# Kernel optimization log

Measured on AMD Instinct MI355X. Metric: run time of the kernel, lower is better.

Reference implementation:

```python
import jax, jax.numpy as jnp
import numpy as np

V, E, H1, H2, Q = 50257, 128, 128, 64, 64
K_BEAM, T_ENC, MAX_LEN = 10, 2048, 30
SOS, EOS, ALPHA = 1, 2, 1.2
NEG = -1e30


def setup_inputs() -> dict:
    key = jax.random.key(0)
    ks = jax.random.split(key, 16)
    s = 0.05  # scale params so logits stay well-conditioned
    emb = jax.random.normal(ks[3], (V, E), jnp.float32) * s
    emb = emb.at[EOS].set(0.0)  # padding_idx=<eos> row is zeros
    return {
        'enc_key': jax.random.normal(ks[0], (T_ENC, 1, Q), jnp.float32),
        'enc_values': jax.random.normal(ks[1], (T_ENC, 1, Q), jnp.float32),
        'mask': jnp.ones((1, 1, T_ENC), jnp.float32),
        'embedding': emb,
        'W_ih1': jax.random.normal(ks[4], (4 * H1, E + Q), jnp.float32) * s,
        'W_hh1': jax.random.normal(ks[5], (4 * H1, H1), jnp.float32) * s,
        'b_ih1': jax.random.normal(ks[6], (4 * H1,), jnp.float32) * s,
        'b_hh1': jax.random.normal(ks[7], (4 * H1,), jnp.float32) * s,
        'W_ih2': jax.random.normal(ks[8], (4 * H2, H1), jnp.float32) * s,
        'W_hh2': jax.random.normal(ks[9], (4 * H2, H2), jnp.float32) * s,
        'b_ih2': jax.random.normal(ks[10], (4 * H2,), jnp.float32) * s,
        'b_hh2': jax.random.normal(ks[11], (4 * H2,), jnp.float32) * s,
        'Wq': jax.random.normal(ks[12], (Q, H2), jnp.float32) * s,
        'bq': jax.random.normal(ks[13], (Q,), jnp.float32) * s,
        'Wc': jax.random.normal(ks[14], (V, H2 + Q), jnp.float32) * s,
        'bc': jax.random.normal(ks[15], (V,), jnp.float32) * s,
    }


def _lstm_cell(x, h, c, Wih, Whh, bih, bhh):
    # torch LSTMCell gate order: i, f, g, o
    g = x @ Wih.T + bih + h @ Whh.T + bhh
    i, f, gg, o = jnp.split(g, 4, axis=-1)
    c = jax.nn.sigmoid(f) * c + jax.nn.sigmoid(i) * jnp.tanh(gg)
    h = jax.nn.sigmoid(o) * jnp.tanh(c)
    return h, c


def beam_search(enc_key, enc_values, mask, embedding, W_ih1, W_hh1, b_ih1, b_hh1,
                W_ih2, W_hh2, b_ih2, b_hh2, Wq, bq, Wc, bc):
    k = K_BEAM
    key_t = jnp.transpose(jnp.broadcast_to(enc_key, (T_ENC, k, Q)), (1, 0, 2))    # [k,T,Q]
    val_t = jnp.transpose(jnp.broadcast_to(enc_values, (T_ENC, k, Q)), (1, 0, 2))  # [k,T,Q]
    m = jnp.broadcast_to(mask[:, 0, :], (k, T_ENC))                                # [k,T]
    eos_row = jnp.where(jnp.arange(V) == EOS, 0.0, NEG)  # finished beams: force <eos> at logp 0
    beam_ids = jnp.arange(k)

    carry0 = (jnp.full((k,), SOS, jnp.int32),      # prev words
              jnp.zeros((k,), jnp.float32),        # cumulative scores
              jnp.zeros((k, H1)), jnp.zeros((k, H1)),  # lstm1 h,c
              jnp.zeros((k, H2)), jnp.zeros((k, H2)),  # lstm2 h,c
              jnp.zeros((k, Q)),                   # attention context
              jnp.zeros((k,), bool),               # finished mask
              jnp.full((k, MAX_LEN + 1), SOS, jnp.int32))  # seqs buffer

    def step(carry, i):
        prev, scores, h1, c1, h2, c2, ctx, fin, seqs = carry
        emb = embedding[prev]                                   # [k,E]
        h1, c1 = _lstm_cell(jnp.concatenate([emb, ctx], -1), h1, c1, W_ih1, W_hh1, b_ih1, b_hh1)
        h2, c2 = _lstm_cell(h1, h2, c2, W_ih2, W_hh2, b_ih2, b_hh2)
        q = h2 @ Wq.T + bq                                       # [k,Q]
        energy = jnp.einsum('kq,ktq->kt', q, key_t)              # [k,T]
        att = jax.nn.softmax(energy, axis=1)
        matt = m * att
        matt = matt / jnp.clip(matt.sum(axis=1, keepdims=True), 2e-30)
        ctx = jnp.einsum('kt,ktv->kv', matt, val_t)              # [k,Q]
        logits = jnp.concatenate([h2, ctx], -1) @ Wc.T + bc      # [k,V]
        logp = jax.nn.log_softmax(logits, axis=1)
        logp = jnp.where(fin[:, None], eos_row[None, :], logp)
        cand = scores[:, None] + logp                            # [k,V]
        # step 0: all beams identical -> only expand beam 0 (matches scores[0].topk)
        cand = jnp.where((i == 0) & (beam_ids[:, None] > 0), NEG, cand)
        top_scores, top_idx = jax.lax.top_k(cand.reshape(-1), k)
        prev_beam = top_idx // V
        nxt = (top_idx % V).astype(jnp.int32)
        h1, c1, h2, c2, ctx = (a[prev_beam] for a in (h1, c1, h2, c2, ctx))
        seqs = seqs[prev_beam].at[:, i + 1].set(nxt)
        fin = fin[prev_beam] | (nxt == EOS)
        return (nxt, top_scores, h1, c1, h2, c2, ctx, fin, seqs), None

    carry, _ = jax.lax.scan(step, carry0, jnp.arange(MAX_LEN))
    _, scores, _, _, _, _, _, _, seqs = carry
    is_eos = seqs[:, 1:] == EOS
    has_eos = is_eos.any(axis=1)
    first = jnp.argmax(is_eos, axis=1)
    # length = tokens incl. <sos> and <eos> (forced <eos> appended if never produced)
    length = jnp.where(has_eos, first + 2, MAX_LEN + 2).astype(jnp.float32)
    norm_scores = scores / (length ** ALPHA)
    return seqs, scores, norm_scores


def reference(enc_key, enc_values, mask, embedding, W_ih1, W_hh1, b_ih1, b_hh1,
              W_ih2, W_hh2, b_ih2, b_hh2, Wq, bq, Wc, bc):
    return beam_search(enc_key, enc_values, mask, embedding, W_ih1, W_hh1, b_ih1, b_hh1,
                       W_ih2, W_hh2, b_ih2, b_hh2, Wq, bq, Wc, bc)
```

## Files before the change

kernel.cpp:

```cpp
#include <hip/hip_runtime.h>
#include <math.h>

#define K_BEAM  10
#define V_SZ    50257
#define E_SZ    128
#define H1_SZ   128
#define H2_SZ   64
#define Q_SZ    64
#define T_SZ    2048
#define MAXLEN  30
#define SEQ_LEN 31
#define SOS_TOK 1
#define EOS_TOK 2

#define NBLK 256
#define NTHR 512
#define VC   197
#define XSTR 132

#define ST_A_F   0
#define ST_B_F   8960
#define SD_H1    0
#define SD_C1    1280
#define SD_H2    2560
#define SD_C2    3200
#define SD_CTX   3840
#define META_A_F 17920
#define META_B_F 18272
#define M_SC     0
#define M_FIN    20
#define M_PREV   30
#define M_SEQ    40
#define XS_F     19936
#define LSEM_F   83136
#define LSES_F   88256
#define CANDV_F  93376
#define CANDI_F  118976
#define B10V_F   144576
#define B10F_F   144776

__device__ __forceinline__ void wave_merge_ms_d(double& m, double& s) {
  #pragma unroll
  for (int off = 32; off > 0; off >>= 1) {
    double om = __shfl_down(m, off, 64);
    double os = __shfl_down(s, off, 64);
    double nm = fmax(m, om);
    s = s * exp(m - nm) + os * exp(om - nm);
    m = nm;
  }
}
__device__ __forceinline__ void wave_argmax_f(float& v, int& i) {
  #pragma unroll
  for (int off = 32; off > 0; off >>= 1) {
    float ov = __shfl_down(v, off, 64);
    int   oi = __shfl_down(i, off, 64);
    if (ov > v || (ov == v && oi < i)) { v = ov; i = oi; }
  }
}

__device__ __forceinline__ void merge100(const float* ws, double* selv, int* self_, int lane) {
  const double* bv = (const double*)(ws + B10V_F);
  const int*    bf = (const int*)(ws + B10F_F);
  double av = (lane < 100) ? bv[lane] : -1e302;
  int    af = (lane < 100) ? bf[lane] : 0x7fffffff;
  const int c1 = lane + 64;
  double cv = (c1 < 100) ? bv[c1] : -1e302;
  int    cf = (c1 < 100) ? bf[c1] : 0x7fffffff;
  #pragma unroll
  for (int pick = 0; pick < 10; ++pick) {
    bool tb = (cv > av) || (cv == av && cf < af);
    double lv = tb ? cv : av;
    int    lf = tb ? cf : af;
    int    ls = tb ? c1 : lane;
    #pragma unroll
    for (int off = 32; off > 0; off >>= 1) {
      double ov = __shfl_down(lv, off, 64);
      int    of = __shfl_down(lf, off, 64);
      int    os = __shfl_down(ls, off, 64);
      if (ov > lv || (ov == lv && of < lf)) { lv = ov; lf = of; ls = os; }
    }
    ls = __shfl(ls, 0, 64);
    if (lane == 0) { selv[pick] = lv; self_[pick] = lf; }
    if (ls == lane) { av = -1e302; af = 0x7fffffff; }
    if (ls == c1)   { cv = -1e302; cf = 0x7fffffff; }
  }
}

__global__ __launch_bounds__(NTHR, 2) void stepA_kernel(
    float* __restrict__ ws, int step,
    const float* __restrict__ embedding,
    const float* __restrict__ W_ih1, const float* __restrict__ W_hh1,
    const float* __restrict__ b_ih1, const float* __restrict__ b_hh1,
    const float* __restrict__ W_ih2, const float* __restrict__ W_hh2,
    const float* __restrict__ b_ih2, const float* __restrict__ b_hh2,
    const float* __restrict__ Wq, const float* __restrict__ bq,
    const float* __restrict__ enc_key, const float* __restrict__ enc_values,
    const float* __restrict__ maskp)
{
  const int blk = blockIdx.x;
  if (blk & 7) return;
  const int b = blk >> 3;

  const int tid  = threadIdx.x;
  const int lane = tid & 63;
  const int wv   = tid >> 6;

  __shared__ double sh_e[T_SZ];
  __shared__ double sh_red[NTHR];
  __shared__ double sh_xin[192];
  __shared__ double sh_h1p[128];
  __shared__ double sh_g1[512];
  __shared__ double sh_h1n[128];
  __shared__ double sh_h2p[64];
  __shared__ double sh_gt2[256];
  __shared__ double sh_h2n[64];
  __shared__ double sh_qs[64];
  __shared__ double sh_selv[10];
  __shared__ int    sh_self[10];
  __shared__ int    sh_pb, sh_tok;

  const int par = step & 1;
  const double* S = (const double*)(ws + (par == 0 ? ST_A_F : ST_B_F));
  double*       D = (double*)(ws + (par == 0 ? ST_B_F : ST_A_F));
  const float* msrc = ws + (par == 0 ? META_A_F : META_B_F);
  float*       mdst = ws + (par == 0 ? META_B_F : META_A_F);

  if (step == 0) {
    double* SA = (double*)(ws + ST_A_F);
    if (tid < 128) { SA[SD_H1 + b*H1_SZ + tid] = 0.0; SA[SD_C1 + b*H1_SZ + tid] = 0.0; }
    if (tid >= 128 && tid < 192) {
      int i2 = tid - 128;
      SA[SD_H2 + b*H2_SZ + i2] = 0.0; SA[SD_C2 + b*H2_SZ + i2] = 0.0;
      SA[SD_CTX + b*Q_SZ + i2] = 0.0;
    }
    float* mA = ws + META_A_F;
    if (tid == 0) {
      ((double*)(mA + M_SC))[b] = 0.0;
      ((int*)(mA + M_FIN))[b] = 0;
      ((int*)(mA + M_PREV))[b] = SOS_TOK;
    }
    if (tid < SEQ_LEN) ((int*)(mA + M_SEQ))[b*SEQ_LEN + tid] = SOS_TOK;
    __syncthreads();
  }

  if (step == 0) {
    if (tid == 0) {
      int tok = ((const int*)(msrc + M_PREV))[b];
      double sc = ((const double*)(msrc + M_SC))[b];
      int fin = ((const int*)(msrc + M_FIN))[b];
      sh_pb = b; sh_tok = tok;
      ((double*)(mdst + M_SC))[b] = sc;
      ((int*)(mdst + M_FIN))[b] = fin;
      ((int*)(mdst + M_PREV))[b] = tok;
    }
  } else {
    if (wv == 0) merge100(ws, sh_selv, sh_self, lane);
    __syncthreads();
    if (tid == 0) {
      int f = sh_self[b];
      int pb = f / V_SZ; int tok = f - pb*V_SZ;
      pb = min(max(pb, 0), K_BEAM - 1); tok = min(max(tok, 0), V_SZ - 1);
      double sc = sh_selv[b];
      int fin = ((const int*)(msrc + M_FIN))[pb] | (tok == EOS_TOK);
      sh_pb = pb; sh_tok = tok;
      ((double*)(mdst + M_SC))[b] = sc;
      ((int*)(mdst + M_FIN))[b] = fin;
      ((int*)(mdst + M_PREV))[b] = tok;
    }
  }
  __syncthreads();
  const int pb = sh_pb, tok = sh_tok;

  if (tid < SEQ_LEN) {
    int v = ((const int*)(msrc + M_SEQ))[pb*SEQ_LEN + tid];
    if (step > 0 && tid == step) v = tok;
    ((int*)(mdst + M_SEQ))[b*SEQ_LEN + tid] = v;
  }
  if (tid < 128)                     sh_xin[tid] = (double)embedding[(size_t)tok*E_SZ + tid];
  else if (tid < 192)                sh_xin[tid] = S[SD_CTX + pb*Q_SZ + (tid - 128)];
  if (tid >= 256 && tid < 384)       sh_h1p[tid - 256] = S[SD_H1 + pb*H1_SZ + (tid - 256)];
  __syncthreads();

  {
    const int r = tid;
    double acc = (double)b_ih1[r] + (double)b_hh1[r];
    const float4* wi = (const float4*)(W_ih1 + (size_t)r*192);
    float4 st[12];
    for (int j0 = 0; j0 < 48; j0 += 12) {
      #pragma unroll
      for (int u = 0; u < 12; ++u) st[u] = wi[j0 + u];
      #pragma unroll
      for (int u = 0; u < 12; ++u) {
        const int j = j0 + u;
        acc += (double)st[u].x*sh_xin[4*j]   + (double)st[u].y*sh_xin[4*j+1]
             + (double)st[u].z*sh_xin[4*j+2] + (double)st[u].w*sh_xin[4*j+3];
      }
    }
    const float4* wh = (const float4*)(W_hh1 + (size_t)r*128);
    for (int j0 = 0; j0 < 32; j0 += 8) {
      #pragma unroll
      for (int u = 0; u < 8; ++u) st[u] = wh[j0 + u];
      #pragma unroll
      for (int u = 0; u < 8; ++u) {
        const int j = j0 + u;
        acc += (double)st[u].x*sh_h1p[4*j]   + (double)st[u].y*sh_h1p[4*j+1]
             + (double)st[u].z*sh_h1p[4*j+2] + (double)st[u].w*sh_h1p[4*j+3];
      }
    }
    sh_g1[r] = acc;
  }
  __syncthreads();
  if (tid < 128) {
    double ig = 1.0/(1.0 + exp(-sh_g1[tid]));
    double fg = 1.0/(1.0 + exp(-sh_g1[128 + tid]));
    double gg = tanh(sh_g1[256 + tid]);
    double og = 1.0/(1.0 + exp(-sh_g1[384 + tid]));
    double c = fg * S[SD_C1 + pb*H1_SZ + tid] + ig*gg;
    double h = og * tanh(c);
    D[SD_C1 + b*H1_SZ + tid] = c; D[SD_H1 + b*H1_SZ + tid] = h;
    sh_h1n[tid] = h;
  }
  if (tid >= 128 && tid < 192) sh_h2p[tid - 128] = S[SD_H2 + pb*H2_SZ + (tid - 128)];
  __syncthreads();

  if (tid < 256) {
    const int r = tid;
    double acc = (double)b_ih2[r] + (double)b_hh2[r];
    const float4* wi2 = (const float4*)(W_ih2 + (size_t)r*128);
    float4 st[8];
    for (int j0 = 0; j0 < 32; j0 += 8) {
      #pragma unroll
      for (int u = 0; u < 8; ++u) st[u] = wi2[j0 + u];
      #pragma unroll
      for (int u = 0; u < 8; ++u) {
        const int j = j0 + u;
        acc += (double)st[u].x*sh_h1n[4*j]   + (double)st[u].y*sh_h1n[4*j+1]
             + (double)st[u].z*sh_h1n[4*j+2] + (double)st[u].w*sh_h1n[4*j+3];
      }
    }
    const float4* wh2 = (const float4*)(W_hh2 + (size_t)r*64);
    for (int j0 = 0; j0 < 16; j0 += 8) {
      #pragma unroll
      for (int u = 0; u < 8; ++u) st[u] = wh2[j0 + u];
      #pragma unroll
      for (int u = 0; u < 8; ++u) {
        const int j = j0 + u;
        acc += (double)st[u].x*sh_h2p[4*j]   + (double)st[u].y*sh_h2p[4*j+1]
             + (double)st[u].z*sh_h2p[4*j+2] + (double)st[u].w*sh_h2p[4*j+3];
      }
    }
    sh_gt2[r] = acc;
  }
  __syncthreads();
  if (tid < 64) {
    double ig = 1.0/(1.0 + exp(-sh_gt2[tid]));
    double fg = 1.0/(1.0 + exp(-sh_gt2[64 + tid]));
    double gg = tanh(sh_gt2[128 + tid]);
    double og = 1.0/(1.0 + exp(-sh_gt2[192 + tid]));
    double c = fg * S[SD_C2 + pb*H2_SZ + tid] + ig*gg;
    double h = og * tanh(c);
    D[SD_C2 + b*H2_SZ + tid] = c; D[SD_H2 + b*H2_SZ + tid] = h;
    sh_h2n[tid] = h;
    ((double*)(ws + XS_F))[b*128 + tid] = h;
  }
  __syncthreads();
  if (tid < 64) {
    double acc = (double)bq[tid];
    const float4* wr = (const float4*)(Wq + (size_t)tid*64);
    float4 st[16];
    #pragma unroll
    for (int u = 0; u < 16; ++u) st[u] = wr[u];
    #pragma unroll
    for (int j = 0; j < 16; ++j) {
      acc += (double)st[j].x*sh_h2n[4*j]   + (double)st[j].y*sh_h2n[4*j+1]
           + (double)st[j].z*sh_h2n[4*j+2] + (double)st[j].w*sh_h2n[4*j+3];
    }
    sh_qs[tid] = acc;
  }
  __syncthreads();

  double lmax = -1e300;
  for (int t = tid; t < T_SZ; t += NTHR) {
    const float4* kr = (const float4*)(enc_key + (size_t)t*64);
    float4 st[16];
    #pragma unroll
    for (int u = 0; u < 16; ++u) st[u] = kr[u];
    double e = 0.0;
    #pragma unroll
    for (int j = 0; j < 16; ++j) {
      e += (double)st[j].x*sh_qs[4*j]   + (double)st[j].y*sh_qs[4*j+1]
         + (double)st[j].z*sh_qs[4*j+2] + (double)st[j].w*sh_qs[4*j+3];
    }
    sh_e[t] = e;
    lmax = fmax(lmax, e);
  }
  sh_red[tid] = lmax; __syncthreads();
  for (int s2 = 256; s2 > 0; s2 >>= 1) { if (tid < s2) sh_red[tid] = fmax(sh_red[tid], sh_red[tid + s2]); __syncthreads(); }
  const double mx = sh_red[0]; __syncthreads();
  double lsum = 0.0;
  for (int t = tid; t < T_SZ; t += NTHR) lsum += exp(sh_e[t] - mx);
  sh_red[tid] = lsum; __syncthreads();
  for (int s2 = 256; s2 > 0; s2 >>= 1) { if (tid < s2) sh_red[tid] += sh_red[tid + s2]; __syncthreads(); }
  const double Ss = sh_red[0]; __syncthreads();
  double lms = 0.0;
  for (int t = tid; t < T_SZ; t += NTHR) {
    double w = (double)maskp[t] * (exp(sh_e[t] - mx) / Ss);
    sh_e[t] = w;
    lms += w;
  }
  sh_red[tid] = lms; __syncthreads();
  for (int s2 = 256; s2 > 0; s2 >>= 1) { if (tid < s2) sh_red[tid] += sh_red[tid + s2]; __syncthreads(); }
  const double ms = fmax(sh_red[0], 2e-30); __syncthreads();
  {
    const int v = tid & 63, g = tid >> 6;
    double acc = 0.0;
    float ev[8];
    for (int k0 = 0; k0 < 256; k0 += 8) {
      #pragma unroll
      for (int u = 0; u < 8; ++u)
        ev[u] = enc_values[(size_t)(g + 8*(k0 + u))*64 + v];
      #pragma unroll
      for (int u = 0; u < 8; ++u)
        acc += sh_e[g + 8*(k0 + u)] * (double)ev[u];
    }
    sh_red[tid] = acc;
  }
  __syncthreads();
  if (tid < 64) {
    double cv = 0.0;
    #pragma unroll
    for (int g = 0; g < 8; ++g) cv += sh_red[g*64 + tid];
    cv /= ms;
    D[SD_CTX + b*Q_SZ + tid] = cv;
    ((double*)(ws + XS_F))[b*128 + 64 + tid] = cv;
  }
}

__global__ __launch_bounds__(NTHR, 2) void stepB_kernel(
    float* __restrict__ ws, int step,
    const float* __restrict__ Wc, const float* __restrict__ bc)
{
  const int tid  = threadIdx.x;
  const int blk  = blockIdx.x;
  const int lane = tid & 63;
  const int wv   = tid >> 6;

  __shared__ double sh_xs[K_BEAM*XSTR];
  __shared__ float  sh_lg[VC*K_BEAM];

  const int v0 = blk * VC;
  const int vn = min(VC, V_SZ - v0);

  for (int i2 = tid; i2 < K_BEAM*128; i2 += NTHR) {
    int b2 = i2 >> 7, j = i2 & 127;
    sh_xs[b2*XSTR + j] = ((const double*)(ws + XS_F))[i2];
  }
  __syncthreads();

  {
    const int g = lane >> 3, k = lane & 7;
    for (int r0 = wv * 8; r0 < vn; r0 += 64) {
      const int r = r0 + g;
      const bool act = (r < vn);
      float4 rw0, rw1, rw2, rw3;
      double bcv = 0.0;
      if (act) {
        const float4* wr4 = (const float4*)(Wc + (size_t)(v0 + r)*128);
        rw0 = wr4[k]; rw1 = wr4[k + 8]; rw2 = wr4[k + 16]; rw3 = wr4[k + 24];
        bcv = (double)bc[v0 + r];
      } else {
        rw0 = rw1 = rw2 = rw3 = make_float4(0.f, 0.f, 0.f, 0.f);
      }
      #pragma unroll 1
      for (int b2 = 0; b2 < K_BEAM; ++b2) {
        const double* xb = &sh_xs[b2*XSTR];
        double p = 0.0;
        {
          const double* xp = xb + (k + 0)*4;
          p += (double)rw0.x*xp[0]; p += (double)rw0.y*xp[1];
          p += (double)rw0.z*xp[2]; p += (double)rw0.w*xp[3];
        }
        {
          const double* xp = xb + (k + 8)*4;
          p += (double)rw1.x*xp[0]; p += (double)rw1.y*xp[1];
          p += (double)rw1.z*xp[2]; p += (double)rw1.w*xp[3];
        }
        {
          const double* xp = xb + (k + 16)*4;
          p += (double)rw2.x*xp[0]; p += (double)rw2.y*xp[1];
          p += (double)rw2.z*xp[2]; p += (double)rw2.w*xp[3];
        }
        {
          const double* xp = xb + (k + 24)*4;
          p += (double)rw3.x*xp[0]; p += (double)rw3.y*xp[1];
          p += (double)rw3.z*xp[2]; p += (double)rw3.w*xp[3];
        }
        p += __shfl_xor(p, 1, 64);
        p += __shfl_xor(p, 2, 64);
        p += __shfl_xor(p, 4, 64);
        if (act && k == 0) sh_lg[r*K_BEAM + b2] = (float)(p + bcv);
      }
    }
  }
  __syncthreads();

  {
    double* lse_m = (double*)(ws + LSEM_F);
    double* lse_s = (double*)(ws + LSES_F);
    float*  cvv   = ws + CANDV_F;
    int*    cii   = (int*)(ws + CANDI_F);
    for (int b2 = wv; b2 < K_BEAM; b2 += 8) {
      double m = -1e300, s = 0.0;
      for (int vl = lane; vl < vn; vl += 64) {
        double val = (double)sh_lg[vl*K_BEAM + b2];
        double nm = fmax(m, val);
        s = s*exp(m - nm) + exp(val - nm); m = nm;
      }
      wave_merge_ms_d(m, s);
      if (lane == 0) { lse_m[blk*K_BEAM + b2] = m; lse_s[blk*K_BEAM + b2] = s; }
      #pragma unroll
      for (int pick = 0; pick < 10; ++pick) {
        float bv = -3e38f; int bi = 0x7ffffff0;
        for (int vl = lane; vl < vn; vl += 64) {
          float val = sh_lg[vl*K_BEAM + b2];
          if (val > bv || (val == bv && vl < bi)) { bv = val; bi = vl; }
        }
        wave_argmax_f(bv, bi);
        bv = __shfl(bv, 0, 64); bi = __shfl(bi, 0, 64);
        int wi = min(max(bi, 0), vn - 1);
        if (lane == 0) {
          cvv[(blk*K_BEAM + b2)*10 + pick] = bv;
          cii[(blk*K_BEAM + b2)*10 + pick] = v0 + wi;
        }
        if (bi >= 0 && bi < vn && (bi & 63) == lane) sh_lg[bi*K_BEAM + b2] = -3e38f;
      }
    }
  }
}

__global__ __launch_bounds__(NTHR) void stepC_kernel(float* __restrict__ ws, int step)
{
  const int tid  = threadIdx.x;
  const int j    = blockIdx.x;
  const int lane = tid & 63;
  const int wv   = tid >> 6;

  __shared__ double sh_wtv[80];
  __shared__ int    sh_wti[80];
  __shared__ double sh_base;

  const int par = step & 1;
  const float* mcur = ws + (par == 0 ? META_B_F : META_A_F);
  const double scj = ((const double*)(mcur + M_SC))[j];
  const int finj   = ((const int*)(mcur + M_FIN))[j];
  const bool masked = finj || (step == 0 && j > 0);

  if (wv == 0) {
    double m = -1e300, s = 0.0;
    for (int c = lane; c < NBLK; c += 64) {
      double mc  = ((const double*)(ws + LSEM_F))[c*K_BEAM + j];
      double sc2 = ((const double*)(ws + LSES_F))[c*K_BEAM + j];
      double nm = fmax(m, mc);
      s = s*exp(m - nm) + sc2*exp(mc - nm); m = nm;
    }
    wave_merge_ms_d(m, s);
    if (lane == 0) sh_base = scj - (m + log(s));
  }
  __syncthreads();
  const double base = sh_base;

  float rv[5]; int ri[5];
  #pragma unroll
  for (int k = 0; k < 5; ++k) {
    int c = wv*320 + 64*k + lane;
    int blkc = c / 10, p = c - blkc*10;
    int idx = (blkc*K_BEAM + j)*10 + p;
    rv[k] = (ws + CANDV_F)[idx];
    ri[k] = ((const int*)(ws + CANDI_F))[idx];
  }
  #pragma unroll
  for (int pick = 0; pick < 10; ++pick) {
    double lv = -1e301; int li = 0x7ffffff0;
    if (!masked) {
      #pragma unroll
      for (int k = 0; k < 5; ++k) {
        double val = base + (double)rv[k];
        int v = ri[k];
        if (val > lv || (val == lv && v < li)) { lv = val; li = v; }
      }
    }
    #pragma unroll
    for (int off = 32; off > 0; off >>= 1) {
      double ov = __shfl_down(lv, off, 64);
      int    oi = __shfl_down(li, off, 64);
      if (ov > lv || (ov == lv && oi < li)) { lv = ov; li = oi; }
    }
    lv = __shfl(lv, 0, 64); li = __shfl(li, 0, 64);
    if (!masked) {
      #pragma unroll
      for (int k = 0; k < 5; ++k) if (ri[k] == li) rv[k] = -3e38f;
    }
    if (lane == 0) { sh_wtv[wv*10 + pick] = lv; sh_wti[wv*10 + pick] = li; }
  }
  __syncthreads();

  if (wv == 0) {
    double av = (lane < 80) ? sh_wtv[lane] : -1e305;
    int    ai = (lane < 80) ? sh_wti[lane] : 0x7fffffff;
    const int c1 = lane + 64;
    double bv2 = (c1 < 80) ? sh_wtv[c1] : -1e305;
    int    bi2 = (c1 < 80) ? sh_wti[c1] : 0x7fffffff;
    #pragma unroll
    for (int pick = 0; pick < 10; ++pick) {
      bool tb = (bv2 > av) || (bv2 == av && bi2 < ai);
      double lv = tb ? bv2 : av;
      int    li = tb ? bi2 : ai;
      int    ls = tb ? c1  : lane;
      #pragma unroll
      for (int off = 32; off > 0; off >>= 1) {
        double ov = __shfl_down(lv, off, 64);
        int    oi = __shfl_down(li, off, 64);
        int    os = __shfl_down(ls, off, 64);
        if (ov > lv || (ov == lv && oi < li)) { lv = ov; li = oi; ls = os; }
      }
      ls = __shfl(ls, 0, 64);
      if (ls == lane) { av  = -1e305; ai  = 0x7fffffff; }
      if (ls == c1)   { bv2 = -1e305; bi2 = 0x7fffffff; }
      if (lane == 0) {
        double outv; int outf;
        if (finj) {
          outv = (pick == 0) ? scj : -1e301;
          outf = (pick == 0) ? (j*V_SZ + EOS_TOK) : 0x7ffffff0;
        } else if (step == 0 && j > 0) {
          outv = -1e301; outf = 0x7ffffff0;
        } else {
          outv = lv;
          outf = j*V_SZ + min(max(li, 0), V_SZ - 1);
        }
        ((double*)(ws + B10V_F))[j*10 + pick] = outv;
        ((int*)(ws + B10F_F))[j*10 + pick] = outf;
      }
    }
  }
}

__global__ __launch_bounds__(NTHR) void final_kernel(float* __restrict__ ws,
                                                     float* __restrict__ out)
{
  const int tid  = threadIdx.x;
  const int lane = tid & 63;
  const int wv   = tid >> 6;
  __shared__ double sh_selv[10];
  __shared__ int    sh_self[10];
  __shared__ int    sh_seqF[K_BEAM*SEQ_LEN];
  __shared__ int    sh_fpb[K_BEAM], sh_ftok[K_BEAM];

  if (wv == 0) merge100(ws, sh_selv, sh_self, lane);
  __syncthreads();
  const float* mA = ws + META_A_F;
  const int* seqA = (const int*)(mA + M_SEQ);
  if (tid < K_BEAM) {
    int f = sh_self[tid];
    int pb = f / V_SZ, tk2 = f - pb*V_SZ;
    sh_fpb[tid]  = min(max(pb, 0), K_BEAM - 1);
    sh_ftok[tid] = min(max(tk2, 0), V_SZ - 1);
  }
  __syncthreads();
  for (int t = tid; t < K_BEAM*SEQ_LEN; t += NTHR) {
    int j2 = t / SEQ_LEN, p = t - j2*SEQ_LEN;
    sh_seqF[t] = (p == MAXLEN) ? sh_ftok[j2] : seqA[sh_fpb[j2]*SEQ_LEN + p];
  }
  __syncthreads();
  if (tid < K_BEAM) {
    int first = -1;
    for (int p = 1; p <= MAXLEN; ++p)
      if (sh_seqF[tid*SEQ_LEN + p] == EOS_TOK) { first = p - 1; break; }
    double len = (first >= 0) ? (double)(first + 2) : (double)(MAXLEN + 2);
    double scv = sh_selv[tid];
    out[K_BEAM*SEQ_LEN + tid] = (float)scv;
    out[K_BEAM*SEQ_LEN + K_BEAM + tid] = (float)(scv / pow(len, 1.2));
  }
  for (int t = tid; t < K_BEAM*SEQ_LEN; t += NTHR) out[t] = (float)sh_seqF[t];
}

extern "C" void kernel_launch(void* const* d_in, const int* in_sizes, int n_in,
                              void* d_out, int out_size, void* d_ws, size_t ws_size,
                              hipStream_t stream) {
  (void)in_sizes; (void)n_in; (void)out_size; (void)ws_size;
  const float* enc_key    = (const float*)d_in[0];
  const float* enc_values = (const float*)d_in[1];
  const float* maskp      = (const float*)d_in[2];
  const float* embedding  = (const float*)d_in[3];
  const float* W_ih1      = (const float*)d_in[4];
  const float* W_hh1      = (const float*)d_in[5];
  const float* b_ih1      = (const float*)d_in[6];
  const float* b_hh1      = (const float*)d_in[7];
  const float* W_ih2      = (const float*)d_in[8];
  const float* W_hh2      = (const float*)d_in[9];
  const float* b_ih2      = (const float*)d_in[10];
  const float* b_hh2      = (const float*)d_in[11];
  const float* Wq         = (const float*)d_in[12];
  const float* bq         = (const float*)d_in[13];
  const float* Wc         = (const float*)d_in[14];
  const float* bc         = (const float*)d_in[15];
  float* ws  = (float*)d_ws;
  float* out = (float*)d_out;

  for (int i = 0; i < MAXLEN; ++i) {
    stepA_kernel<<<8*K_BEAM, NTHR, 0, stream>>>(ws, i, embedding,
        W_ih1, W_hh1, b_ih1, b_hh1, W_ih2, W_hh2, b_ih2, b_hh2,
        Wq, bq, enc_key, enc_values, maskp);
    stepB_kernel<<<NBLK, NTHR, 0, stream>>>(ws, i, Wc, bc);
    stepC_kernel<<<K_BEAM, NTHR, 0, stream>>>(ws, i);
  }
  final_kernel<<<1, NTHR, 0, stream>>>(ws, out);
}
```

Baseline: 3.810 ms.

## Split attention into energy and context kernels across 80 blocks per step

The attention part of stepA used to run on only 10 active blocks, one per beam, each looping over all 2048 encoder positions. It now runs as two kernels, energy and ctx, each over 80 blocks that handle 256-position chunks. Chunk softmax statistics are combined online, and stepB adds up the partial context vectors and normalises them. This spreads the attention work over more CUs, at the cost of two extra kernel launches per step and extra workspace round-trips.

```diff
diff --git a/kernel.cpp b/kernel.cpp
--- a/kernel.cpp
+++ b/kernel.cpp
@@ -38,6 +38,12 @@
 #define CANDI_F  118976
 #define B10V_F   144576
 #define B10F_F   144776
+#define QD_F     150016
+#define ENG_F    151296
+#define MC_F     192256
+#define SCC_F    192416
+#define MSC_F    192576
+#define CTXC_F   192736
 
 __device__ __forceinline__ void wave_merge_ms_d(double& m, double& s) {
   #pragma unroll
@@ -86,16 +92,14 @@
   }
 }
 
-__global__ __launch_bounds__(NTHR, 2) void stepA_kernel(
+__global__ __launch_bounds__(NTHR, 2) void stepA1_kernel(
     float* __restrict__ ws, int step,
     const float* __restrict__ embedding,
     const float* __restrict__ W_ih1, const float* __restrict__ W_hh1,
     const float* __restrict__ b_ih1, const float* __restrict__ b_hh1,
     const float* __restrict__ W_ih2, const float* __restrict__ W_hh2,
     const float* __restrict__ b_ih2, const float* __restrict__ b_hh2,
-    const float* __restrict__ Wq, const float* __restrict__ bq,
-    const float* __restrict__ enc_key, const float* __restrict__ enc_values,
-    const float* __restrict__ maskp)
+    const float* __restrict__ Wq, const float* __restrict__ bq)
 {
   const int blk = blockIdx.x;
   if (blk & 7) return;
@@ -105,8 +109,6 @@
   const int lane = tid & 63;
   const int wv   = tid >> 6;
 
-  __shared__ double sh_e[T_SZ];
-  __shared__ double sh_red[NTHR];
   __shared__ double sh_xin[192];
   __shared__ double sh_h1p[128];
   __shared__ double sh_g1[512];
@@ -114,7 +116,6 @@
   __shared__ double sh_h2p[64];
   __shared__ double sh_gt2[256];
   __shared__ double sh_h2n[64];
-  __shared__ double sh_qs[64];
   __shared__ double sh_selv[10];
   __shared__ int    sh_self[10];
   __shared__ int    sh_pb, sh_tok;
@@ -275,65 +276,95 @@
       acc += (double)st[j].x*sh_h2n[4*j]   + (double)st[j].y*sh_h2n[4*j+1]
            + (double)st[j].z*sh_h2n[4*j+2] + (double)st[j].w*sh_h2n[4*j+3];
     }
-    sh_qs[tid] = acc;
-  }
-  __syncthreads();
-
-  double lmax = -1e300;
-  for (int t = tid; t < T_SZ; t += NTHR) {
-    const float4* kr = (const float4*)(enc_key + (size_t)t*64);
-    float4 st[16];
+    ((double*)(ws + QD_F))[b*64 + tid] = acc;
+  }
+}
+
+__global__ __launch_bounds__(256, 2) void energy_kernel(
+    float* __restrict__ ws, const float* __restrict__ enc_key)
+{
+  const int tid = threadIdx.x;
+  const int bm = blockIdx.x >> 3, ch = blockIdx.x & 7;
+  __shared__ double qs[64], rm[256], rs[256];
+  if (tid < 64) qs[tid] = ((const double*)(ws + QD_F))[bm*64 + tid];
+  __syncthreads();
+  const int t = ch*256 + tid;
+  const float4* kr = (const float4*)(enc_key + (size_t)t*64);
+  float4 st[16];
+  #pragma unroll
+  for (int u = 0; u < 16; ++u) st[u] = kr[u];
+  double e = 0.0;
+  #pragma unroll
+  for (int j = 0; j < 16; ++j) {
+    e += (double)st[j].x*qs[4*j]   + (double)st[j].y*qs[4*j+1]
+       + (double)st[j].z*qs[4*j+2] + (double)st[j].w*qs[4*j+3];
+  }
+  ((double*)(ws + ENG_F))[bm*2048 + t] = e;
+  rm[tid] = e; rs[tid] = 1.0;
+  __syncthreads();
+  for (int s2 = 128; s2 > 0; s2 >>= 1) {
+    if (tid < s2) {
+      double m1 = rm[tid], m2 = rm[tid + s2];
+      double nm = fmax(m1, m2);
+      rs[tid] = rs[tid]*exp(m1 - nm) + rs[tid + s2]*exp(m2 - nm);
+      rm[tid] = nm;
+    }
+    __syncthreads();
+  }
+  if (tid == 0) {
+    ((double*)(ws + MC_F))[bm*8 + ch]  = rm[0];
+    ((double*)(ws + SCC_F))[bm*8 + ch] = rs[0];
+  }
+}
+
+__global__ __launch_bounds__(256, 2) void ctx_kernel(
+    float* __restrict__ ws, const float* __restrict__ enc_values,
+    const float* __restrict__ maskp)
+{
+  const int tid = threadIdx.x;
+  const int bm = blockIdx.x >> 3, ch = blockIdx.x & 7;
+  __shared__ double e_s[256], red[256];
+  __shared__ float  m_s[256];
+  __shared__ double mxS, SsS;
+  e_s[tid] = ((const double*)(ws + ENG_F))[bm*2048 + ch*256 + tid];
+  m_s[tid] = maskp[ch*256 + tid];
+  if (tid == 0) {
+    double m = -1e300, s = 0.0;
+    for (int c = 0; c < 8; ++c) {
+      double mc = ((const double*)(ws + MC_F))[bm*8 + c];
+      double sc = ((const double*)(ws + SCC_F))[bm*8 + c];
+      double nm = fmax(m, mc);
+      s = s*exp(m - nm) + sc*exp(mc - nm);
+      m = nm;
+    }
+    mxS = m; SsS = s;
+  }
+  __syncthreads();
+  const double mx = mxS, Ss = SsS;
+  double matt = (double)m_s[tid] * (exp(e_s[tid] - mx)/Ss);
+  red[tid] = matt; __syncthreads();
+  for (int s2 = 128; s2 > 0; s2 >>= 1) { if (tid < s2) red[tid] += red[tid + s2]; __syncthreads(); }
+  if (tid == 0) ((double*)(ws + MSC_F))[bm*8 + ch] = red[0];
+  __syncthreads();
+  const int v = tid & 63, g4 = tid >> 6;
+  double acc = 0.0;
+  float ev[16];
+  for (int k0 = 0; k0 < 64; k0 += 16) {
     #pragma unroll
-    for (int u = 0; u < 16; ++u) st[u] = kr[u];
-    double e = 0.0;
+    for (int u = 0; u < 16; ++u) {
+      int tl = g4 + 4*(k0 + u);
+      ev[u] = enc_values[(size_t)(ch*256 + tl)*64 + v];
+    }
     #pragma unroll
-    for (int j = 0; j < 16; ++j) {
-      e += (double)st[j].x*sh_qs[4*j]   + (double)st[j].y*sh_qs[4*j+1]
-         + (double)st[j].z*sh_qs[4*j+2] + (double)st[j].w*sh_qs[4*j+3];
-    }
-    sh_e[t] = e;
-    lmax = fmax(lmax, e);
-  }
-  sh_red[tid] = lmax; __syncthreads();
-  for (int s2 = 256; s2 > 0; s2 >>= 1) { if (tid < s2) sh_red[tid] = fmax(sh_red[tid], sh_red[tid + s2]); __syncthreads(); }
-  const double mx = sh_red[0]; __syncthreads();
-  double lsum = 0.0;
-  for (int t = tid; t < T_SZ; t += NTHR) lsum += exp(sh_e[t] - mx);
-  sh_red[tid] = lsum; __syncthreads();
-  for (int s2 = 256; s2 > 0; s2 >>= 1) { if (tid < s2) sh_red[tid] += sh_red[tid + s2]; __syncthreads(); }
-  const double Ss = sh_red[0]; __syncthreads();
-  double lms = 0.0;
-  for (int t = tid; t < T_SZ; t += NTHR) {
-    double w = (double)maskp[t] * (exp(sh_e[t] - mx) / Ss);
-    sh_e[t] = w;
-    lms += w;
-  }
-  sh_red[tid] = lms; __syncthreads();
-  for (int s2 = 256; s2 > 0; s2 >>= 1) { if (tid < s2) sh_red[tid] += sh_red[tid + s2]; __syncthreads(); }
-  const double ms = fmax(sh_red[0], 2e-30); __syncthreads();
-  {
-    const int v = tid & 63, g = tid >> 6;
-    double acc = 0.0;
-    float ev[8];
-    for (int k0 = 0; k0 < 256; k0 += 8) {
-      #pragma unroll
-      for (int u = 0; u < 8; ++u)
-        ev[u] = enc_values[(size_t)(g + 8*(k0 + u))*64 + v];
-      #pragma unroll
-      for (int u = 0; u < 8; ++u)
-        acc += sh_e[g + 8*(k0 + u)] * (double)ev[u];
-    }
-    sh_red[tid] = acc;
-  }
-  __syncthreads();
-  if (tid < 64) {
-    double cv = 0.0;
-    #pragma unroll
-    for (int g = 0; g < 8; ++g) cv += sh_red[g*64 + tid];
-    cv /= ms;
-    D[SD_CTX + b*Q_SZ + tid] = cv;
-    ((double*)(ws + XS_F))[b*128 + 64 + tid] = cv;
-  }
+    for (int u = 0; u < 16; ++u) {
+      int tl = g4 + 4*(k0 + u);
+      double mt = (double)m_s[tl] * (exp(e_s[tl] - mx)/Ss);
+      acc += mt * (double)ev[u];
+    }
+  }
+  red[tid] = acc; __syncthreads();
+  if (g4 == 0)
+    ((double*)(ws + CTXC_F))[(bm*8 + ch)*64 + v] = red[v] + red[64+v] + red[128+v] + red[192+v];
 }
 
 __global__ __launch_bounds__(NTHR, 2) void stepB_kernel(
@@ -350,10 +381,20 @@
 
   const int v0 = blk * VC;
   const int vn = min(VC, V_SZ - v0);
-
-  for (int i2 = tid; i2 < K_BEAM*128; i2 += NTHR) {
-    int b2 = i2 >> 7, j = i2 & 127;
-    sh_xs[b2*XSTR + j] = ((const double*)(ws + XS_F))[i2];
+  const int par = step & 1;
+  double* D = (double*)(ws + (par == 0 ? ST_B_F : ST_A_F));
+
+  for (int i2 = tid; i2 < 640; i2 += NTHR) {
+    int b2 = i2 >> 6, v = i2 & 63;
+    sh_xs[b2*XSTR + v] = ((const double*)(ws + XS_F))[b2*128 + v];
+    double msv = 0.0;
+    for (int c = 0; c < 8; ++c) msv += ((const double*)(ws + MSC_F))[b2*8 + c];
+    msv = fmax(msv, 2e-30);
+    double cv = 0.0;
+    for (int c = 0; c < 8; ++c) cv += ((const double*)(ws + CTXC_F))[(b2*8 + c)*64 + v];
+    cv /= msv;
+    sh_xs[b2*XSTR + 64 + v] = cv;
+    if (blk == 0) D[SD_CTX + b2*64 + v] = cv;
   }
   __syncthreads();
 
@@ -607,9 +648,10 @@
   float* out = (float*)d_out;
 
   for (int i = 0; i < MAXLEN; ++i) {
-    stepA_kernel<<<8*K_BEAM, NTHR, 0, stream>>>(ws, i, embedding,
-        W_ih1, W_hh1, b_ih1, b_hh1, W_ih2, W_hh2, b_ih2, b_hh2,
-        Wq, bq, enc_key, enc_values, maskp);
+    stepA1_kernel<<<8*K_BEAM, NTHR, 0, stream>>>(ws, i, embedding,
+        W_ih1, W_hh1, b_ih1, b_hh1, W_ih2, W_hh2, b_ih2, b_hh2, Wq, bq);
+    energy_kernel<<<8*K_BEAM, 256, 0, stream>>>(ws, enc_key);
+    ctx_kernel<<<8*K_BEAM, 256, 0, stream>>>(ws, enc_values, maskp);
     stepB_kernel<<<NBLK, NTHR, 0, stream>>>(ws, i, Wc, bc);
     stepC_kernel<<<K_BEAM, NTHR, 0, stream>>>(ws, i);
   }
```

Result: faster. 3.686 ms (-3.2%).
